# Kernel tuning notes

Measured on AMD Instinct MI355X. Metric: run time of the kernel, lower is better.

Reference implementation:

```python
import jax, jax.numpy as jnp
import numpy as np

H = W = 56
WS = 7          # window size
SHIFT = 3
HEADS = 16
EPS = 1e-5
# padding per SwinMLPBlock: [P_l, P_r, P_t, P_b] = [WS-SHIFT, SHIFT, WS-SHIFT, SHIFT]
P_L, P_R, P_T, P_B = WS - SHIFT, SHIFT, WS - SHIFT, SHIFT


def layer_norm(x, g, b):
    mu = jnp.mean(x, axis=-1, keepdims=True)
    var = jnp.mean(jnp.square(x - mu), axis=-1, keepdims=True)
    return (x - mu) * jax.lax.rsqrt(var + EPS) * g + b


def setup_inputs() -> dict:
    key = jax.random.key(0)
    ks = jax.random.split(key, 8)
    B, L, C = 32, H * W, 512
    hid = 4 * C
    s = lambda fan: 1.0 / np.sqrt(fan)
    return {
        "x": jax.random.normal(ks[0], (B, L, C), jnp.float32),
        "norm1_g": jnp.ones((C,), jnp.float32),
        "norm1_b": jnp.zeros((C,), jnp.float32),
        "spatial_w": jax.random.normal(ks[1], (HEADS, WS * WS, WS * WS), jnp.float32) * s(WS * WS),
        "spatial_b": jax.random.normal(ks[2], (HEADS, WS * WS), jnp.float32) * 0.02,
        "norm2_g": jnp.ones((C,), jnp.float32),
        "norm2_b": jnp.zeros((C,), jnp.float32),
        "fc1_w": jax.random.normal(ks[3], (hid, C), jnp.float32) * s(C),
        "fc1_b": jnp.zeros((hid,), jnp.float32),
        "fc2_w": jax.random.normal(ks[4], (C, hid), jnp.float32) * s(hid),
        "fc2_b": jnp.zeros((C,), jnp.float32),
    }


def reference(x, norm1_g, norm1_b, spatial_w, spatial_b, norm2_g, norm2_b,
              fc1_w, fc1_b, fc2_w, fc2_b):
    B, L, C = x.shape
    hc = C // HEADS
    shortcut = x

    xn = layer_norm(x, norm1_g, norm1_b).reshape(B, H, W, C)
    # shift via zero pad (shift_size > 0 path)
    xp = jnp.pad(xn, ((0, 0), (P_T, P_B), (P_L, P_R), (0, 0)))
    _H, _W = H + WS, W + WS  # 63, 63

    # window partition -> (B*nW, WS*WS, HEADS, hc) -> (n, HEADS, WS*WS, hc)
    xw = xp.reshape(B, _H // WS, WS, _W // WS, WS, C)
    xw = xw.transpose(0, 1, 3, 2, 4, 5).reshape(-1, WS * WS, HEADS, hc)
    xh = xw.transpose(0, 2, 1, 3)  # (n, heads, ws2, hc)

    # grouped conv1d(kernel=1, groups=heads) == per-head [ws2, ws2] matmul
    yh = jnp.einsum('hij,nhjc->nhic', spatial_w, xh) + spatial_b[None, :, :, None]

    # back to windows, then window reverse
    yw = yh.transpose(0, 2, 1, 3).reshape(-1, WS, WS, C)
    y = yw.reshape(B, _H // WS, _W // WS, WS, WS, C)
    y = y.transpose(0, 1, 3, 2, 4, 5).reshape(B, _H, _W, C)
    y = y[:, P_T:_H - P_B, P_L:_W - P_R, :].reshape(B, L, C)

    x = shortcut + y
    # channel MLP with residual
    xn2 = layer_norm(x, norm2_g, norm2_b)
    h = jax.nn.gelu(xn2 @ fc1_w.T + fc1_b, approximate=False)
    return x + (h @ fc2_w.T + fc2_b)
```

## Files before the change

kernel.cpp:

```cpp
#include <hip/hip_runtime.h>

#define HH 56
#define WW 56
#define CC 512
#define BB 32
#define LL (HH*WW)
#define MM (BB*LL)
#define HID 2048

typedef __attribute__((ext_vector_type(8))) __bf16 bf16x8;
typedef __attribute__((ext_vector_type(4))) float f32x4;
typedef __attribute__((ext_vector_type(4))) short s16x4;

__device__ __forceinline__ short f2bf(float f) {
    union { float f; unsigned u; } c; c.f = f;
    unsigned r = c.u + 0x7fffu + ((c.u >> 16) & 1u);
    return (short)(r >> 16);
}
__device__ __forceinline__ float bf2f(short s) {
    union { unsigned u; float f; } c; c.u = ((unsigned)(unsigned short)s) << 16;
    return c.f;
}

__device__ __forceinline__ float gelu_fast(float v) {
    float xg = 0.7978845608f * (v + 0.044715f * v * v * v);
    xg = fminf(xg, 15.0f);
    float t = __expf(2.0f * xg);
    return v * (t / (t + 1.0f));
}

__global__ __launch_bounds__(256) void cvt_bf16(const float* __restrict__ in,
                                                short* __restrict__ out, int n) {
    int i = blockIdx.x * 256 + threadIdx.x;
    if (i < n) out[i] = f2bf(in[i]);
}

__global__ __launch_bounds__(256) void ln512v(const float* __restrict__ x,
                                              const float* __restrict__ g,
                                              const float* __restrict__ b,
                                              short* __restrict__ out) {
    const int t = threadIdx.x;
    const int rsel = t >> 7;
    const int col = t & 127;
    const long row = (long)blockIdx.x * 2 + rsel;
    const f32x4 v = ((const f32x4*)(x + row * 512))[col];
    float s = v[0] + v[1] + v[2] + v[3];
    float q = v[0]*v[0] + v[1]*v[1] + v[2]*v[2] + v[3]*v[3];
#pragma unroll
    for (int off = 32; off > 0; off >>= 1) {
        s += __shfl_xor(s, off, 64);
        q += __shfl_xor(q, off, 64);
    }
    __shared__ float red[8];
    const int wv = t >> 6;
    if ((t & 63) == 0) { red[wv] = s; red[4 + wv] = q; }
    __syncthreads();
    s = red[rsel * 2] + red[rsel * 2 + 1];
    q = red[4 + rsel * 2] + red[4 + rsel * 2 + 1];
    const float mu = s * (1.0f / 512.0f);
    const float rs = rsqrtf(q * (1.0f / 512.0f) - mu * mu + 1e-5f);
    const f32x4 gv = ((const f32x4*)g)[col];
    const f32x4 bv = ((const f32x4*)b)[col];
    s16x4 o;
#pragma unroll
    for (int r = 0; r < 4; ++r)
        o[r] = f2bf((v[r] - mu) * rs * gv[r] + bv[r]);
    *(s16x4*)(out + row * 512 + col * 4) = o;
}

__global__ __launch_bounds__(256) void spatial_mlp(const short* __restrict__ xn,
                                                   const float* __restrict__ x,
                                                   const float* __restrict__ sw,
                                                   const float* __restrict__ sb,
                                                   float* x1) {
    const int head = blockIdx.y;
    const int t = threadIdx.x;
    const int chp = t & 15;
    const int wloc = t >> 4;
    const int win = blockIdx.x * 16 + wloc;
    const int b = win / 81;
    const int rr = win - b * 81;
    const int wi = rr / 9;
    const int wj = rr - wi * 9;
    const int c = head * 32 + chp * 2;

    float2 xv[49];
#pragma unroll
    for (int j = 0; j < 49; j++) {
        const int pr = wi * 7 + j / 7 - 4;
        const int pc = wj * 7 + j % 7 - 4;
        float2 v = {0.0f, 0.0f};
        if (pr >= 0 && pr < 56 && pc >= 0 && pc < 56) {
            const long idx = ((long)((b * 56 + pr) * 56 + pc)) * 512 + c;
            const ushort2 u = *(const ushort2*)(xn + idx);
            v.x = bf2f((short)u.x);
            v.y = bf2f((short)u.y);
        }
        xv[j] = v;
    }

    const float* swh = sw + head * 2401;
    const float* sbh = sb + head * 49;

#pragma unroll 1
    for (int t7 = 0; t7 < 7; t7++) {
        float2 acc[7];
#pragma unroll
        for (int ii = 0; ii < 7; ii++) {
            const float bb = sbh[t7 * 7 + ii];
            acc[ii].x = bb; acc[ii].y = bb;
        }
#pragma unroll
        for (int ii = 0; ii < 7; ii++) {
            const float* swr = swh + (t7 * 7 + ii) * 49;
#pragma unroll
            for (int j = 0; j < 49; j++) {
                acc[ii].x = fmaf(swr[j], xv[j].x, acc[ii].x);
                acc[ii].y = fmaf(swr[j], xv[j].y, acc[ii].y);
            }
        }
        const int pr = wi * 7 + t7 - 4;
        if (pr >= 0 && pr < 56) {
#pragma unroll
            for (int ii = 0; ii < 7; ii++) {
                const int pc = wj * 7 + ii - 4;
                if (pc >= 0 && pc < 56) {
                    const long idx = ((long)((b * 56 + pr) * 56 + pc)) * 512 + c;
                    const float2 rv = *(const float2*)(x + idx);
                    float2 o; o.x = rv.x + acc[ii].x; o.y = rv.y + acc[ii].y;
                    *(float2*)(x1 + idx) = o;
                }
            }
        }
    }
}

template <int K, int N, bool GELU>
__global__ __launch_bounds__(256, 3) void gemm128(const short* __restrict__ A,
                                                  const short* __restrict__ Bw,
                                                  const float* __restrict__ bias,
                                                  const float* res,
                                                  void* Cout) {
    __shared__ __attribute__((aligned(16))) short S[24576];
    const int tid = threadIdx.x;
    const int lane = tid & 63;
    const int wid = tid >> 6;
    const int wr = wid >> 1;
    const int wc = wid & 1;
    const int lr = lane & 15;
    const int kg = (lane >> 4) & 3;

    const int gx = gridDim.x;
    const int lin = blockIdx.y * gx + blockIdx.x;
    const int cpx = (gx * gridDim.y) >> 3;
    const int orig = (lin & 7) * cpx + (lin >> 3);
    const long mBase = (long)(orig / gx) * 128;
    const long nBase = (long)(orig % gx) * 128;

    const int sRow = tid >> 2;
    const int sChunk = (tid & 3) ^ ((tid >> 3) & 3);
    const short* aSrc0 = A + (mBase + sRow) * K + sChunk * 8;
    const short* aSrc1 = A + (mBase + 64 + sRow) * K + sChunk * 8;
    const short* bSrc0 = Bw + (nBase + sRow) * K + sChunk * 8;
    const short* bSrc1 = Bw + (nBase + 64 + sRow) * K + sChunk * 8;

    auto stage = [&](int buf, int t) {
        const long k0 = (long)t * 32;
        char* Ad = (char*)S + buf * 8192 + tid * 16;
        char* Bd = (char*)S + 24576 + buf * 8192 + tid * 16;
        __builtin_amdgcn_global_load_lds(
            (const __attribute__((address_space(1))) void*)(aSrc0 + k0),
            (__attribute__((address_space(3))) void*)Ad, 16, 0, 0);
        __builtin_amdgcn_global_load_lds(
            (const __attribute__((address_space(1))) void*)(aSrc1 + k0),
            (__attribute__((address_space(3))) void*)(Ad + 4096), 16, 0, 0);
        __builtin_amdgcn_global_load_lds(
            (const __attribute__((address_space(1))) void*)(bSrc0 + k0),
            (__attribute__((address_space(3))) void*)Bd, 16, 0, 0);
        __builtin_amdgcn_global_load_lds(
            (const __attribute__((address_space(1))) void*)(bSrc1 + k0),
            (__attribute__((address_space(3))) void*)(Bd + 4096), 16, 0, 0);
    };

    const int swzc = kg ^ ((lr >> 1) & 3);
    const int aOff = (wr * 64 + lr) * 64 + swzc * 16;
    const int bOff = (wc * 64 + lr) * 64 + swzc * 16;

    f32x4 acc[4][4] = {};

    stage(0, 0); stage(1, 1);
    asm volatile("s_waitcnt vmcnt(4)" ::: "memory");
    __builtin_amdgcn_s_barrier();

    const int NT = K / 32;
    int cb = 0;
    for (int t = 0; t < NT; ++t) {
        if (t + 2 < NT) {
            const int sb = cb >= 1 ? cb - 1 : 2;
            stage(sb, t + 2);
        }
        const char* Ab = (const char*)S + cb * 8192;
        const char* Bb = (const char*)S + 24576 + cb * 8192;
        bf16x8 af[4], bf[4];
#pragma unroll
        for (int m = 0; m < 4; ++m) af[m] = *(const bf16x8*)(Ab + aOff + m * 1024);
#pragma unroll
        for (int n = 0; n < 4; ++n) bf[n] = *(const bf16x8*)(Bb + bOff + n * 1024);
        asm volatile("s_waitcnt lgkmcnt(0)" ::: "memory");
        __builtin_amdgcn_s_setprio(1);
#pragma unroll
        for (int m = 0; m < 4; ++m)
#pragma unroll
            for (int n = 0; n < 4; ++n)
                acc[m][n] = __builtin_amdgcn_mfma_f32_16x16x32_bf16(bf[n], af[m],
                                                                    acc[m][n], 0, 0, 0);
        __builtin_amdgcn_s_setprio(0);
        if (t + 1 < NT) {
            if (t + 2 < NT) asm volatile("s_waitcnt vmcnt(4)" ::: "memory");
            else            asm volatile("s_waitcnt vmcnt(0)" ::: "memory");
        }
        __builtin_amdgcn_s_barrier();
        cb = cb + 1 == 3 ? 0 : cb + 1;
    }

#pragma unroll
    for (int n = 0; n < 4; ++n) {
        const long col0 = nBase + wc * 64 + n * 16 + kg * 4;
        const f32x4 bv4 = *(const f32x4*)(bias + col0);
#pragma unroll
        for (int m = 0; m < 4; ++m) {
            const long row = mBase + wr * 64 + m * 16 + lr;
            const long idx = row * N + col0;
            if (GELU) {
                s16x4 o;
#pragma unroll
                for (int r = 0; r < 4; ++r)
                    o[r] = f2bf(gelu_fast(acc[m][n][r] + bv4[r]));
                *(s16x4*)((short*)Cout + idx) = o;
            } else {
                const f32x4 rv = *(const f32x4*)(res + idx);
                f32x4 o;
#pragma unroll
                for (int r = 0; r < 4; ++r) o[r] = acc[m][n][r] + bv4[r] + rv[r];
                *(f32x4*)((float*)Cout + idx) = o;
            }
        }
    }
}

extern "C" void kernel_launch(void* const* d_in, const int* in_sizes, int n_in,
                              void* d_out, int out_size, void* d_ws, size_t ws_size,
                              hipStream_t stream) {
    const float* x    = (const float*)d_in[0];
    const float* n1g  = (const float*)d_in[1];
    const float* n1b  = (const float*)d_in[2];
    const float* sw   = (const float*)d_in[3];
    const float* sb   = (const float*)d_in[4];
    const float* n2g  = (const float*)d_in[5];
    const float* n2b  = (const float*)d_in[6];
    const float* fc1w = (const float*)d_in[7];
    const float* fc1b = (const float*)d_in[8];
    const float* fc2w = (const float*)d_in[9];
    const float* fc2b = (const float*)d_in[10];
    float* out = (float*)d_out;

    char* ws = (char*)d_ws;
    short* xn  = (short*)ws;
    short* hb  = (short*)(ws + 102760448);
    short* w1b = (short*)(ws + 513802240);
    short* w2b = (short*)(ws + 515899392);

    cvt_bf16<<<4096, 256, 0, stream>>>(fc1w, w1b, 2048 * 512);
    cvt_bf16<<<4096, 256, 0, stream>>>(fc2w, w2b, 512 * 2048);

    ln512v<<<MM / 2, 256, 0, stream>>>(x, n1g, n1b, xn);

    spatial_mlp<<<dim3(162, 16), 256, 0, stream>>>(xn, x, sw, sb, out);

    ln512v<<<MM / 2, 256, 0, stream>>>(out, n2g, n2b, xn);

    gemm128<512, 2048, true><<<dim3(16, 784), 256, 0, stream>>>(xn, w1b, fc1b, nullptr, hb);

    gemm128<2048, 512, false><<<dim3(4, 784), 256, 0, stream>>>(hb, w2b, fc2b, out, out);
}
```

Measured before the change: 1.066 ms.

## Stage GEMM tiles through registers with double-buffered LDS instead of direct global-to-LDS loads

The bf16 GEMM mainloop no longer uses the direct global-to-LDS load builtin with a three-stage LDS ring. Each tile is now loaded into registers two steps ahead and written to one of two LDS buffers one step ahead, with the loop unrolled by two so the buffer indices are compile-time constants. LDS shrinks and the swizzle is applied when writing to LDS, which is meant to cut LDS footprint and the explicit vmcnt waits. The cost is extra VGPRs for the staged tiles, explicit LDS store instructions, and compiler-placed waits on the global loads.

```diff
diff --git a/kernel.cpp b/kernel.cpp
--- a/kernel.cpp
+++ b/kernel.cpp
@@ -136,12 +136,12 @@
 }
 
 template <int K, int N, bool GELU>
-__global__ __launch_bounds__(256, 3) void gemm128(const short* __restrict__ A,
-                                                  const short* __restrict__ Bw,
-                                                  const float* __restrict__ bias,
-                                                  const float* res,
-                                                  void* Cout) {
-    __shared__ __attribute__((aligned(16))) short S[24576];
+__global__ __launch_bounds__(256, 3) void gemmrs(const short* __restrict__ A,
+                                                 const short* __restrict__ Bw,
+                                                 const float* __restrict__ bias,
+                                                 const float* res,
+                                                 void* Cout) {
+    __shared__ __attribute__((aligned(16))) char S[32768];
     const int tid = threadIdx.x;
     const int lane = tid & 63;
     const int wid = tid >> 6;
@@ -158,70 +158,73 @@
     const long nBase = (long)(orig % gx) * 128;
 
     const int sRow = tid >> 2;
-    const int sChunk = (tid & 3) ^ ((tid >> 3) & 3);
-    const short* aSrc0 = A + (mBase + sRow) * K + sChunk * 8;
-    const short* aSrc1 = A + (mBase + 64 + sRow) * K + sChunk * 8;
-    const short* bSrc0 = Bw + (nBase + sRow) * K + sChunk * 8;
-    const short* bSrc1 = Bw + (nBase + 64 + sRow) * K + sChunk * 8;
-
-    auto stage = [&](int buf, int t) {
-        const long k0 = (long)t * 32;
-        char* Ad = (char*)S + buf * 8192 + tid * 16;
-        char* Bd = (char*)S + 24576 + buf * 8192 + tid * 16;
-        __builtin_amdgcn_global_load_lds(
-            (const __attribute__((address_space(1))) void*)(aSrc0 + k0),
-            (__attribute__((address_space(3))) void*)Ad, 16, 0, 0);
-        __builtin_amdgcn_global_load_lds(
-            (const __attribute__((address_space(1))) void*)(aSrc1 + k0),
-            (__attribute__((address_space(3))) void*)(Ad + 4096), 16, 0, 0);
-        __builtin_amdgcn_global_load_lds(
-            (const __attribute__((address_space(1))) void*)(bSrc0 + k0),
-            (__attribute__((address_space(3))) void*)Bd, 16, 0, 0);
-        __builtin_amdgcn_global_load_lds(
-            (const __attribute__((address_space(1))) void*)(bSrc1 + k0),
-            (__attribute__((address_space(3))) void*)(Bd + 4096), 16, 0, 0);
-    };
+    const short* aSrc0 = A + (mBase + sRow) * K + (tid & 3) * 8;
+    const short* aSrc1 = A + (mBase + 64 + sRow) * K + (tid & 3) * 8;
+    const short* bSrc0 = Bw + (nBase + sRow) * K + (tid & 3) * 8;
+    const short* bSrc1 = Bw + (nBase + 64 + sRow) * K + (tid & 3) * 8;
+
+    const int wByte = sRow * 64 + (((tid & 3) ^ ((tid >> 3) & 3)) << 4);
 
     const int swzc = kg ^ ((lr >> 1) & 3);
     const int aOff = (wr * 64 + lr) * 64 + swzc * 16;
     const int bOff = (wc * 64 + lr) * 64 + swzc * 16;
 
     f32x4 acc[4][4] = {};
-
-    stage(0, 0); stage(1, 1);
-    asm volatile("s_waitcnt vmcnt(4)" ::: "memory");
+    const int NT = K / 32;
+    static_assert((K / 32) % 2 == 0, "NT even");
+
+    f32x4 rA00, rA01, rB00, rB01;
+    f32x4 rA10, rA11, rB10, rB11;
+
+#define LOADBANK(P, T) do {                                                     \
+        const long k0_ = (long)(T) * 32;                                        \
+        rA##P##0 = *(const f32x4*)(aSrc0 + k0_);                                \
+        rA##P##1 = *(const f32x4*)(aSrc1 + k0_);                                \
+        rB##P##0 = *(const f32x4*)(bSrc0 + k0_);                                \
+        rB##P##1 = *(const f32x4*)(bSrc1 + k0_);                                \
+    } while (0)
+
+#define WRITEBANK(P) do {                                                       \
+        *(f32x4*)(S + (P) * 8192 + wByte)          = rA##P##0;                  \
+        *(f32x4*)(S + (P) * 8192 + 4096 + wByte)   = rA##P##1;                  \
+        *(f32x4*)(S + 16384 + (P) * 8192 + wByte)        = rB##P##0;            \
+        *(f32x4*)(S + 16384 + (P) * 8192 + 4096 + wByte) = rB##P##1;            \
+    } while (0)
+
+#define BODY(P, Q, T) do {                                                      \
+        if ((T) + 2 < NT) LOADBANK(P, (T) + 2);                                 \
+        if ((T) + 1 < NT) WRITEBANK(Q);                                         \
+        const char* Ab_ = S + (P) * 8192;                                       \
+        const char* Bb_ = S + 16384 + (P) * 8192;                               \
+        bf16x8 af[4], bfv[4];                                                   \
+        _Pragma("unroll")                                                       \
+        for (int m = 0; m < 4; ++m) af[m] = *(const bf16x8*)(Ab_ + aOff + m * 1024); \
+        _Pragma("unroll")                                                       \
+        for (int n = 0; n < 4; ++n) bfv[n] = *(const bf16x8*)(Bb_ + bOff + n * 1024); \
+        asm volatile("s_waitcnt lgkmcnt(0)" ::: "memory");                      \
+        __builtin_amdgcn_s_setprio(1);                                          \
+        _Pragma("unroll")                                                       \
+        for (int m = 0; m < 4; ++m)                                             \
+            _Pragma("unroll")                                                   \
+            for (int n = 0; n < 4; ++n)                                         \
+                acc[m][n] = __builtin_amdgcn_mfma_f32_16x16x32_bf16(bfv[n], af[m], acc[m][n], 0, 0, 0); \
+        __builtin_amdgcn_s_setprio(0);                                          \
+        __builtin_amdgcn_s_barrier();                                           \
+    } while (0)
+
+    LOADBANK(0, 0);
+    LOADBANK(1, 1);
+    WRITEBANK(0);
+    asm volatile("s_waitcnt lgkmcnt(0)" ::: "memory");
     __builtin_amdgcn_s_barrier();
 
-    const int NT = K / 32;
-    int cb = 0;
-    for (int t = 0; t < NT; ++t) {
-        if (t + 2 < NT) {
-            const int sb = cb >= 1 ? cb - 1 : 2;
-            stage(sb, t + 2);
-        }
-        const char* Ab = (const char*)S + cb * 8192;
-        const char* Bb = (const char*)S + 24576 + cb * 8192;
-        bf16x8 af[4], bf[4];
-#pragma unroll
-        for (int m = 0; m < 4; ++m) af[m] = *(const bf16x8*)(Ab + aOff + m * 1024);
-#pragma unroll
-        for (int n = 0; n < 4; ++n) bf[n] = *(const bf16x8*)(Bb + bOff + n * 1024);
-        asm volatile("s_waitcnt lgkmcnt(0)" ::: "memory");
-        __builtin_amdgcn_s_setprio(1);
-#pragma unroll
-        for (int m = 0; m < 4; ++m)
-#pragma unroll
-            for (int n = 0; n < 4; ++n)
-                acc[m][n] = __builtin_amdgcn_mfma_f32_16x16x32_bf16(bf[n], af[m],
-                                                                    acc[m][n], 0, 0, 0);
-        __builtin_amdgcn_s_setprio(0);
-        if (t + 1 < NT) {
-            if (t + 2 < NT) asm volatile("s_waitcnt vmcnt(4)" ::: "memory");
-            else            asm volatile("s_waitcnt vmcnt(0)" ::: "memory");
-        }
-        __builtin_amdgcn_s_barrier();
-        cb = cb + 1 == 3 ? 0 : cb + 1;
-    }
+    for (int t = 0; t < NT; t += 2) {
+        BODY(0, 1, t);
+        BODY(1, 0, t + 1);
+    }
+#undef BODY
+#undef WRITEBANK
+#undef LOADBANK
 
 #pragma unroll
     for (int n = 0; n < 4; ++n) {
@@ -279,7 +282,7 @@
 
     ln512v<<<MM / 2, 256, 0, stream>>>(out, n2g, n2b, xn);
 
-    gemm128<512, 2048, true><<<dim3(16, 784), 256, 0, stream>>>(xn, w1b, fc1b, nullptr, hb);
-
-    gemm128<2048, 512, false><<<dim3(4, 784), 256, 0, stream>>>(hb, w2b, fc2b, out, out);
-}
+    gemmrs<512, 2048, true><<<dim3(16, 784), 256, 0, stream>>>(xn, w1b, fc1b, nullptr, hb);
+
+    gemmrs<2048, 512, false><<<dim3(4, 784), 256, 0, stream>>>(hb, w2b, fc2b, out, out);
+}
```

After: 1.080 ms. About the same (+1.3%).

## Enlarge GEMM tiles to 256x128 and simplify GELU evaluation

Applied to the files above, without the earlier changes.

The MLP GEMMs now use a 256x128 block tile, with each wave holding an 8x4 grid of MFMA accumulators. This raises arithmetic intensity per LDS load and halves the number of blocks, at the cost of more LDS and registers, so occupancy drops to 2 blocks per CU. The tanh-based GELU is refactored into a polynomial form with a fast reciprocal to cut ALU work in the epilogue.

```diff
diff --git a/kernel.cpp b/kernel.cpp
--- a/kernel.cpp
+++ b/kernel.cpp
@@ -23,10 +23,11 @@
 }
 
 __device__ __forceinline__ float gelu_fast(float v) {
-    float xg = 0.7978845608f * (v + 0.044715f * v * v * v);
-    xg = fminf(xg, 15.0f);
-    float t = __expf(2.0f * xg);
-    return v * (t / (t + 1.0f));
+    const float t0 = v * v;
+    const float p = fmaf(t0, 0.08943f, 1.59577f);
+    float xg = fminf(v * p, 30.0f);
+    const float e = __expf(xg);
+    return v * (e * __frcp_rn(e + 1.0f));
 }
 
 __global__ __launch_bounds__(256) void cvt_bf16(const float* __restrict__ in,
@@ -136,12 +137,12 @@
 }
 
 template <int K, int N, bool GELU>
-__global__ __launch_bounds__(256, 3) void gemm128(const short* __restrict__ A,
-                                                  const short* __restrict__ Bw,
-                                                  const float* __restrict__ bias,
-                                                  const float* res,
-                                                  void* Cout) {
-    __shared__ __attribute__((aligned(16))) short S[24576];
+__global__ __launch_bounds__(256, 2) void gemm2x(const short* __restrict__ A,
+                                                 const short* __restrict__ Bw,
+                                                 const float* __restrict__ bias,
+                                                 const float* res,
+                                                 void* Cout) {
+    __shared__ __attribute__((aligned(16))) short S[36864];
     const int tid = threadIdx.x;
     const int lane = tid & 63;
     const int wid = tid >> 6;
@@ -154,42 +155,38 @@
     const int lin = blockIdx.y * gx + blockIdx.x;
     const int cpx = (gx * gridDim.y) >> 3;
     const int orig = (lin & 7) * cpx + (lin >> 3);
-    const long mBase = (long)(orig / gx) * 128;
+    const long mBase = (long)(orig / gx) * 256;
     const long nBase = (long)(orig % gx) * 128;
 
     const int sRow = tid >> 2;
     const int sChunk = (tid & 3) ^ ((tid >> 3) & 3);
-    const short* aSrc0 = A + (mBase + sRow) * K + sChunk * 8;
-    const short* aSrc1 = A + (mBase + 64 + sRow) * K + sChunk * 8;
-    const short* bSrc0 = Bw + (nBase + sRow) * K + sChunk * 8;
-    const short* bSrc1 = Bw + (nBase + 64 + sRow) * K + sChunk * 8;
-
-    auto stage = [&](int buf, int t) {
+    const short* aS = A + (mBase + sRow) * K + sChunk * 8;
+    const short* bS = Bw + (nBase + sRow) * K + sChunk * 8;
+
+    auto stage = [&](int rbuf, int t) {
         const long k0 = (long)t * 32;
-        char* Ad = (char*)S + buf * 8192 + tid * 16;
-        char* Bd = (char*)S + 24576 + buf * 8192 + tid * 16;
-        __builtin_amdgcn_global_load_lds(
-            (const __attribute__((address_space(1))) void*)(aSrc0 + k0),
-            (__attribute__((address_space(3))) void*)Ad, 16, 0, 0);
-        __builtin_amdgcn_global_load_lds(
-            (const __attribute__((address_space(1))) void*)(aSrc1 + k0),
-            (__attribute__((address_space(3))) void*)(Ad + 4096), 16, 0, 0);
-        __builtin_amdgcn_global_load_lds(
-            (const __attribute__((address_space(1))) void*)(bSrc0 + k0),
-            (__attribute__((address_space(3))) void*)Bd, 16, 0, 0);
-        __builtin_amdgcn_global_load_lds(
-            (const __attribute__((address_space(1))) void*)(bSrc1 + k0),
-            (__attribute__((address_space(3))) void*)(Bd + 4096), 16, 0, 0);
+        char* Ad = (char*)S + rbuf * 16384 + tid * 16;
+        char* Bd = (char*)S + 49152 + rbuf * 8192 + tid * 16;
+#pragma unroll
+        for (int j = 0; j < 4; ++j)
+            __builtin_amdgcn_global_load_lds(
+                (const __attribute__((address_space(1))) void*)(aS + k0 + (long)j * 64 * K),
+                (__attribute__((address_space(3))) void*)(Ad + j * 4096), 16, 0, 0);
+#pragma unroll
+        for (int j = 0; j < 2; ++j)
+            __builtin_amdgcn_global_load_lds(
+                (const __attribute__((address_space(1))) void*)(bS + k0 + (long)j * 64 * K),
+                (__attribute__((address_space(3))) void*)(Bd + j * 4096), 16, 0, 0);
     };
 
-    const int swzc = kg ^ ((lr >> 1) & 3);
-    const int aOff = (wr * 64 + lr) * 64 + swzc * 16;
-    const int bOff = (wc * 64 + lr) * 64 + swzc * 16;
-
-    f32x4 acc[4][4] = {};
+    const int swz = (kg ^ ((lr >> 1) & 3)) * 16;
+    const int aOff = (wr * 128 + lr) * 64 + swz;
+    const int bOff = (wc * 64 + lr) * 64 + swz;
+
+    f32x4 acc[8][4] = {};
 
     stage(0, 0); stage(1, 1);
-    asm volatile("s_waitcnt vmcnt(4)" ::: "memory");
+    asm volatile("s_waitcnt vmcnt(6)" ::: "memory");
     __builtin_amdgcn_s_barrier();
 
     const int NT = K / 32;
@@ -199,26 +196,24 @@
             const int sb = cb >= 1 ? cb - 1 : 2;
             stage(sb, t + 2);
         }
-        const char* Ab = (const char*)S + cb * 8192;
-        const char* Bb = (const char*)S + 24576 + cb * 8192;
-        bf16x8 af[4], bf[4];
-#pragma unroll
-        for (int m = 0; m < 4; ++m) af[m] = *(const bf16x8*)(Ab + aOff + m * 1024);
-#pragma unroll
-        for (int n = 0; n < 4; ++n) bf[n] = *(const bf16x8*)(Bb + bOff + n * 1024);
+        const char* Ab = (const char*)S + cb * 16384;
+        const char* Bb = (const char*)S + 49152 + cb * 8192;
+        bf16x8 af[8], bfv[4];
+#pragma unroll
+        for (int m = 0; m < 8; ++m) af[m] = *(const bf16x8*)(Ab + aOff + m * 1024);
+#pragma unroll
+        for (int n = 0; n < 4; ++n) bfv[n] = *(const bf16x8*)(Bb + bOff + n * 1024);
         asm volatile("s_waitcnt lgkmcnt(0)" ::: "memory");
         __builtin_amdgcn_s_setprio(1);
 #pragma unroll
-        for (int m = 0; m < 4; ++m)
+        for (int m = 0; m < 8; ++m)
 #pragma unroll
             for (int n = 0; n < 4; ++n)
-                acc[m][n] = __builtin_amdgcn_mfma_f32_16x16x32_bf16(bf[n], af[m],
+                acc[m][n] = __builtin_amdgcn_mfma_f32_16x16x32_bf16(bfv[n], af[m],
                                                                     acc[m][n], 0, 0, 0);
         __builtin_amdgcn_s_setprio(0);
-        if (t + 1 < NT) {
-            if (t + 2 < NT) asm volatile("s_waitcnt vmcnt(4)" ::: "memory");
-            else            asm volatile("s_waitcnt vmcnt(0)" ::: "memory");
-        }
+        if (t + 2 < NT)      asm volatile("s_waitcnt vmcnt(6)" ::: "memory");
+        else if (t + 1 < NT) asm volatile("s_waitcnt vmcnt(0)" ::: "memory");
         __builtin_amdgcn_s_barrier();
         cb = cb + 1 == 3 ? 0 : cb + 1;
     }
@@ -228,8 +223,8 @@
         const long col0 = nBase + wc * 64 + n * 16 + kg * 4;
         const f32x4 bv4 = *(const f32x4*)(bias + col0);
 #pragma unroll
-        for (int m = 0; m < 4; ++m) {
-            const long row = mBase + wr * 64 + m * 16 + lr;
+        for (int m = 0; m < 8; ++m) {
+            const long row = mBase + wr * 128 + m * 16 + lr;
             const long idx = row * N + col0;
             if (GELU) {
                 s16x4 o;
@@ -279,7 +274,7 @@
 
     ln512v<<<MM / 2, 256, 0, stream>>>(out, n2g, n2b, xn);
 
-    gemm128<512, 2048, true><<<dim3(16, 784), 256, 0, stream>>>(xn, w1b, fc1b, nullptr, hb);
-
-    gemm128<2048, 512, false><<<dim3(4, 784), 256, 0, stream>>>(hb, w2b, fc2b, out, out);
-}
+    gemm2x<512, 2048, true><<<dim3(16, 392), 256, 0, stream>>>(xn, w1b, fc1b, nullptr, hb);
+
+    gemm2x<2048, 512, false><<<dim3(4, 392), 256, 0, stream>>>(hb, w2b, fc2b, out, out);
+}
```

After: 1.077 ms. Within noise of the previous version (+1.1%).

## Split spatial MLP into interior and boundary window kernels; merge weight conversions

Applied to the files above, without the earlier changes.

The spatial token-mixing kernel is split in two. The 49 interior windows per image use a kernel with no bounds checks and simpler addressing, and a separate kernel handles the 32 boundary windows with the original masked path. The two weight fp32-to-bf16 conversion launches are merged into one, and the GEMM epilogue hoists the bias loads and reorders its loops row-major. This removes branch and predication overhead plus one launch, at the cost of an extra kernel launch for the boundary windows.

```diff
diff --git a/kernel.cpp b/kernel.cpp
--- a/kernel.cpp
+++ b/kernel.cpp
@@ -29,10 +29,13 @@
     return v * (t / (t + 1.0f));
 }
 
-__global__ __launch_bounds__(256) void cvt_bf16(const float* __restrict__ in,
-                                                short* __restrict__ out, int n) {
+__global__ __launch_bounds__(256) void cvt2_bf16(const float* __restrict__ in1,
+                                                 short* __restrict__ out1,
+                                                 const float* __restrict__ in2,
+                                                 short* __restrict__ out2, int n) {
     int i = blockIdx.x * 256 + threadIdx.x;
-    if (i < n) out[i] = f2bf(in[i]);
+    if (i < n) out1[i] = f2bf(in1[i]);
+    else if (i < 2 * n) out2[i - n] = f2bf(in2[i - n]);
 }
 
 __global__ __launch_bounds__(256) void ln512v(const float* __restrict__ x,
@@ -68,7 +71,7 @@
     *(s16x4*)(out + row * 512 + col * 4) = o;
 }
 
-__global__ __launch_bounds__(256) void spatial_mlp(const short* __restrict__ xn,
+__global__ __launch_bounds__(256) void spatial_int(const short* __restrict__ xn,
                                                    const float* __restrict__ x,
                                                    const float* __restrict__ sw,
                                                    const float* __restrict__ sb,
@@ -77,11 +80,71 @@
     const int t = threadIdx.x;
     const int chp = t & 15;
     const int wloc = t >> 4;
-    const int win = blockIdx.x * 16 + wloc;
-    const int b = win / 81;
-    const int rr = win - b * 81;
-    const int wi = rr / 9;
-    const int wj = rr - wi * 9;
+    const int wlin = blockIdx.x * 16 + wloc;
+    const int b = wlin / 49;
+    const int r = wlin - b * 49;
+    const int wi = 1 + r / 7;
+    const int wj = 1 + r - (r / 7) * 7;
+    const int c = head * 32 + chp * 2;
+    const long base = ((long)((b * 56 + wi * 7 - 4) * 56) + (wj * 7 - 4)) * 512 + c;
+
+    float2 xv[49];
+#pragma unroll
+    for (int j = 0; j < 49; j++) {
+        const long idx = base + (long)(j / 7) * (56 * 512) + (j % 7) * 512;
+        const ushort2 u = *(const ushort2*)(xn + idx);
+        xv[j].x = bf2f((short)u.x);
+        xv[j].y = bf2f((short)u.y);
+    }
+
+    const float* swh = sw + head * 2401;
+    const float* sbh = sb + head * 49;
+
+#pragma unroll 1
+    for (int t7 = 0; t7 < 7; t7++) {
+        float2 acc[7];
+#pragma unroll
+        for (int ii = 0; ii < 7; ii++) {
+            const float bb = sbh[t7 * 7 + ii];
+            acc[ii].x = bb; acc[ii].y = bb;
+        }
+#pragma unroll
+        for (int ii = 0; ii < 7; ii++) {
+            const float* swr = swh + (t7 * 7 + ii) * 49;
+#pragma unroll
+            for (int j = 0; j < 49; j++) {
+                acc[ii].x = fmaf(swr[j], xv[j].x, acc[ii].x);
+                acc[ii].y = fmaf(swr[j], xv[j].y, acc[ii].y);
+            }
+        }
+        const long rowbase = base + (long)t7 * (56 * 512);
+#pragma unroll
+        for (int ii = 0; ii < 7; ii++) {
+            const long idx = rowbase + ii * 512;
+            const float2 rv = *(const float2*)(x + idx);
+            float2 o; o.x = rv.x + acc[ii].x; o.y = rv.y + acc[ii].y;
+            *(float2*)(x1 + idx) = o;
+        }
+    }
+}
+
+__global__ __launch_bounds__(256) void spatial_bnd(const short* __restrict__ xn,
+                                                   const float* __restrict__ x,
+                                                   const float* __restrict__ sw,
+                                                   const float* __restrict__ sb,
+                                                   float* x1) {
+    const int head = blockIdx.y;
+    const int t = threadIdx.x;
+    const int chp = t & 15;
+    const int wloc = t >> 4;
+    const int wlin = blockIdx.x * 16 + wloc;
+    const int b = wlin >> 5;
+    const int r = wlin & 31;
+    int wi, wj;
+    if (r < 9)       { wi = 0;      wj = r;      }
+    else if (r < 18) { wi = 8;      wj = r - 9;  }
+    else if (r < 25) { wi = r - 17; wj = 0;      }
+    else             { wi = r - 24; wj = 8;      }
     const int c = head * 32 + chp * 2;
 
     float2 xv[49];
@@ -223,25 +286,28 @@
         cb = cb + 1 == 3 ? 0 : cb + 1;
     }
 
-#pragma unroll
-    for (int n = 0; n < 4; ++n) {
-        const long col0 = nBase + wc * 64 + n * 16 + kg * 4;
-        const f32x4 bv4 = *(const f32x4*)(bias + col0);
-#pragma unroll
-        for (int m = 0; m < 4; ++m) {
-            const long row = mBase + wr * 64 + m * 16 + lr;
-            const long idx = row * N + col0;
+    f32x4 bv4[4];
+#pragma unroll
+    for (int n = 0; n < 4; ++n)
+        bv4[n] = *(const f32x4*)(bias + nBase + wc * 64 + n * 16 + kg * 4);
+#pragma unroll
+    for (int m = 0; m < 4; ++m) {
+        const long row = mBase + wr * 64 + m * 16 + lr;
+        const long rowbase = row * N + nBase + wc * 64 + kg * 4;
+#pragma unroll
+        for (int n = 0; n < 4; ++n) {
+            const long idx = rowbase + n * 16;
             if (GELU) {
                 s16x4 o;
 #pragma unroll
                 for (int r = 0; r < 4; ++r)
-                    o[r] = f2bf(gelu_fast(acc[m][n][r] + bv4[r]));
+                    o[r] = f2bf(gelu_fast(acc[m][n][r] + bv4[n][r]));
                 *(s16x4*)((short*)Cout + idx) = o;
             } else {
                 const f32x4 rv = *(const f32x4*)(res + idx);
                 f32x4 o;
 #pragma unroll
-                for (int r = 0; r < 4; ++r) o[r] = acc[m][n][r] + bv4[r] + rv[r];
+                for (int r = 0; r < 4; ++r) o[r] = acc[m][n][r] + bv4[n][r] + rv[r];
                 *(f32x4*)((float*)Cout + idx) = o;
             }
         }
@@ -270,12 +336,12 @@
     short* w1b = (short*)(ws + 513802240);
     short* w2b = (short*)(ws + 515899392);
 
-    cvt_bf16<<<4096, 256, 0, stream>>>(fc1w, w1b, 2048 * 512);
-    cvt_bf16<<<4096, 256, 0, stream>>>(fc2w, w2b, 512 * 2048);
+    cvt2_bf16<<<8192, 256, 0, stream>>>(fc1w, w1b, fc2w, w2b, 2048 * 512);
 
     ln512v<<<MM / 2, 256, 0, stream>>>(x, n1g, n1b, xn);
 
-    spatial_mlp<<<dim3(162, 16), 256, 0, stream>>>(xn, x, sw, sb, out);
+    spatial_int<<<dim3(98, 16), 256, 0, stream>>>(xn, x, sw, sb, out);
+    spatial_bnd<<<dim3(64, 16), 256, 0, stream>>>(xn, x, sw, sb, out);
 
     ln512v<<<MM / 2, 256, 0, stream>>>(out, n2g, n2b, xn);
 
```

After: 976.3 us. 1.09x faster.
